# Kernel optimization log

Hardware: AMD Instinct MI355X
Metric: run time of the kernel (lower is better)

Reference implementation:

```python
import jax, jax.numpy as jnp
import numpy as np

E = 384        # number of edges
HID = 128      # hidden_dim
NH = 8         # num_heads
DH = HID // NH # head_dim = 16
NR = 64        # num_radial
CUTOFF = 10.0
AIN = 2 * DH + NR + 1  # attention MLP input dim = 97


def _xavier(key, fan_in, fan_out):
    a = np.sqrt(6.0 / (fan_in + fan_out))
    return jax.random.uniform(key, (fan_in, fan_out), jnp.float32, -a, a)


def setup_inputs() -> dict:
    key = jax.random.key(0)
    ks = jax.random.split(key, 16)
    return {
        "edge_features": jax.random.normal(ks[0], (E, HID), jnp.float32),
        "edge_coords": jax.random.normal(ks[1], (E, 3), jnp.float32),
        "edge_mask": jnp.zeros((E, E), jnp.float32),  # 0 = connected
        "wq": _xavier(ks[2], HID, HID),
        "wk": _xavier(ks[3], HID, HID),
        "wv": _xavier(ks[4], HID, HID),
        "rbf_centers": jnp.linspace(0.0, CUTOFF, NR).astype(jnp.float32),
        "rbf_widths": jnp.full((NR,), 0.5, jnp.float32),
        "a_w1": _xavier(ks[5], AIN, HID), "a_b1": jnp.zeros((HID,), jnp.float32),
        "a_w2": _xavier(ks[6], HID, HID), "a_b2": jnp.zeros((HID,), jnp.float32),
        "a_w3": _xavier(ks[7], HID, NH),  "a_b3": jnp.zeros((NH,), jnp.float32),
        "g_w1": _xavier(ks[8], DH, HID),  "g_b1": jnp.zeros((HID,), jnp.float32),
        "g_w2": _xavier(ks[9], HID, 1),   "g_b2": jnp.zeros((1,), jnp.float32),
        "wo": _xavier(ks[10], HID, HID),  "bo": jnp.zeros((HID,), jnp.float32),
        "ln_g": jnp.ones((HID,), jnp.float32),
        "ln_b": jnp.zeros((HID,), jnp.float32),
        "edge_index": jax.random.randint(ks[11], (2, E), 0, E, jnp.int64) if jax.config.jax_enable_x64 else jax.random.randint(ks[11], (2, E), 0, E, jnp.int32),
    }


def reference(edge_features, edge_coords, edge_mask,
              wq, wk, wv, rbf_centers, rbf_widths,
              a_w1, a_b1, a_w2, a_b2, a_w3, a_b3,
              g_w1, g_b1, g_w2, g_b2, wo, bo, ln_g, ln_b,
              edge_index):
    silu = jax.nn.silu
    n = edge_features.shape[0]

    q = (edge_features @ wq).reshape(n, NH, DH)
    k = (edge_features @ wk).reshape(n, NH, DH)
    v = (edge_features @ wv).reshape(n, NH, DH)

    # pairwise geometry [E, E, ...]
    coord_diff = edge_coords[:, None, :] - edge_coords[None, :, :]
    dist = jnp.linalg.norm(coord_diff, axis=-1) + 1e-8
    dist = jnp.clip(dist, 1e-8, 1e8)
    dot = jnp.clip(jnp.sum(edge_coords[:, None, :] * edge_coords[None, :, :], -1),
                   -1e8, 1e8)
    d = dist[..., None]                               # [E, E, 1]
    rbf = jnp.exp(-rbf_widths * (d - rbf_centers) ** 2) * (d <= CUTOFF).astype(jnp.float32)

    feats = []
    coords = edge_coords
    for h in range(NH):  # structural loop over fixed num_heads
        qh = jnp.broadcast_to(q[:, h, None, :], (n, n, DH))
        kh = jnp.broadcast_to(k[None, :, h, :], (n, n, DH))
        ai = jnp.concatenate([qh, kh, rbf, dot[..., None]], -1)  # [E, E, 97]
        x = silu(ai @ a_w1 + a_b1)
        x = silu(x @ a_w2 + a_b2)
        scores = (x @ a_w3 + a_b3)[:, :, h] + edge_mask
        scores = jnp.clip(scores, -1e9, 1e9)
        attn = jax.nn.softmax(scores, axis=-1)
        attn = jnp.nan_to_num(attn, nan=0.0, posinf=1.0, neginf=0.0)
        vh = v[:, h, :]
        feats.append(attn @ vh)
        # coord gate from v_head of the query edge, broadcast over keys
        gates = jax.nn.sigmoid(silu(vh @ g_w1 + g_b1) @ g_w2 + g_b2)  # [E, 1]
        coords = coords + jnp.einsum('ij,ijc->ic', attn * gates, coord_diff) / NH

    upd = jnp.concatenate(feats, -1)             # [E, hidden]
    y = edge_features + upd @ wo + bo            # residual + out_proj
    mu = jnp.mean(y, -1, keepdims=True)
    var = jnp.var(y, -1, keepdims=True)
    out_f = (y - mu) / jnp.sqrt(var + 1e-5) * ln_g + ln_b
    return out_f, coords
```

## Files before the change

kernel.cpp:

```cpp
#include <hip/hip_runtime.h>
#include <hip/hip_bf16.h>

#define N 384
#define HIDN 128
#define NHD 8
#define DHD 16
#define NRB 64
#define CUTF 10.0f

#define WS_V 0
#define WS_QPB (WS_V + N*HIDN)
#define WS_KPB (WS_QPB + N*NHD*HIDN/2)
#define WS_GATE (WS_KPB + N*NHD*HIDN/2)
#define WS_UPD (WS_GATE + N*NHD)
#define WS_SCORES (WS_UPD + N*HIDN)

typedef short bf16x8 __attribute__((ext_vector_type(8)));
typedef float floatx4 __attribute__((ext_vector_type(4)));
#define MFMA16(a, b, c) __builtin_amdgcn_mfma_f32_16x16x32_bf16(a, b, c, 0, 0, 0)

__device__ __forceinline__ float siluf(float x) { return x / (1.0f + __expf(-x)); }
__device__ __forceinline__ float silu_fast(float x) {
    return x * __builtin_amdgcn_rcpf(1.0f + __expf(-x));
}
__device__ __forceinline__ short f2bf(float f) {
    unsigned int b = __float_as_uint(f);
    unsigned int r = (b + 0x7fffu + ((b >> 16) & 1u)) >> 16;
    return (short)r;
}
__device__ __forceinline__ float bf2f(short s) {
    return __uint_as_float(((unsigned int)(unsigned short)s) << 16);
}
__device__ __forceinline__ float wave_sum(float v) {
    for (int o = 32; o; o >>= 1) v += __shfl_down(v, o, 64);
    return v;
}

__global__ __launch_bounds__(128) void k_pre(const float* __restrict__ ef,
    const float* __restrict__ wq, const float* __restrict__ wk, const float* __restrict__ wv,
    const float* __restrict__ aw1,
    const float* __restrict__ gw1, const float* __restrict__ gb1,
    const float* __restrict__ gw2, const float* __restrict__ gb2,
    float* __restrict__ v, unsigned short* __restrict__ Qpb,
    unsigned short* __restrict__ Kpb, float* __restrict__ gates) {
    __shared__ float sE[HIDN], sQ[HIDN], sK[HIDN], sV[HIDN];
    __shared__ float sRed[2];
    int i = blockIdx.x, t = threadIdx.x;
    sE[t] = ef[i * HIDN + t];
    __syncthreads();
    float aq = 0.f, ak = 0.f, av = 0.f;
#pragma unroll 8
    for (int c = 0; c < HIDN; c++) {
        float e = sE[c];
        aq += e * wq[c * HIDN + t];
        ak += e * wk[c * HIDN + t];
        av += e * wv[c * HIDN + t];
    }
    v[i * HIDN + t] = av;
    sQ[t] = aq; sK[t] = ak; sV[t] = av;
    __syncthreads();
    for (int h = 0; h < NHD; h++) {
        float accq = 0.f, acck = 0.f;
#pragma unroll
        for (int d = 0; d < DHD; d++) {
            accq += sQ[h * DHD + d] * aw1[d * HIDN + t];
            acck += sK[h * DHD + d] * aw1[(DHD + d) * HIDN + t];
        }
        Qpb[(i * NHD + h) * HIDN + t] = (unsigned short)f2bf(accq);
        Kpb[(i * NHD + h) * HIDN + t] = (unsigned short)f2bf(acck);
        float tt = gb1[t];
#pragma unroll
        for (int d = 0; d < DHD; d++) tt += sV[h * DHD + d] * gw1[d * HIDN + t];
        float contrib = siluf(tt) * gw2[t];
        float s = wave_sum(contrib);
        if ((t & 63) == 0) sRed[t >> 6] = s;
        __syncthreads();
        if (t == 0) gates[i * NHD + h] = 1.0f / (1.0f + __expf(-(sRed[0] + sRed[1] + gb2[0])));
        __syncthreads();
    }
}

#define OFF_W1RT 0
#define OFF_QPB  18432
#define OFF_W3T  20480
#define OFF_B1   24576
#define OFF_W1D  25088
#define OFF_B2   25600
#define OFF_AB3  26112
#define OFF_SDD  26144
#define OFF_RBF  26272
#define OFF_R    28576
#define SMEM_SZ  37024
#define OFF_STAGE 0

__global__ __launch_bounds__(256, 2) void k_scores_mfma(
    const float* __restrict__ coords, const float* __restrict__ mask,
    const float* __restrict__ centers, const float* __restrict__ widths,
    const float* __restrict__ aw1, const float* __restrict__ ab1,
    const float* __restrict__ aw2, const float* __restrict__ ab2,
    const float* __restrict__ aw3, const float* __restrict__ ab3,
    const unsigned short* __restrict__ Qpb, const unsigned short* __restrict__ Kpb,
    float* __restrict__ scores) {
    __shared__ __align__(16) char smem[SMEM_SZ];
    const int t = threadIdx.x;
    const int lane = t & 63;
    const int w = t >> 6;
    const int l15 = lane & 15;
    const int quad = lane >> 4;
    const int i = blockIdx.y;
    const int jb = blockIdx.x * 128;

    for (int idx = t; idx < HIDN * HIDN; idx += 256) {
        int k = idx >> 7, n = idx & 127;
        *(short*)(smem + OFF_STAGE + n * 272 + k * 2) = f2bf(aw2[idx]);
    }
    __syncthreads();
    bf16x8 BW2[8][4];
#pragma unroll
    for (int ct = 0; ct < 8; ct++)
#pragma unroll
        for (int ks = 0; ks < 4; ks++)
            BW2[ct][ks] = *(const bf16x8*)(smem + OFF_STAGE + (ct * 16 + l15) * 272 + ks * 64 + quad * 16);
    __syncthreads();
    for (int idx = t; idx < NRB * HIDN; idx += 256) {
        int r = idx >> 7, n = idx & 127;
        *(short*)(smem + OFF_W1RT + n * 144 + r * 2) = f2bf(aw1[32 * HIDN + idx]);
    }
    {
        const unsigned int* qsrc = (const unsigned int*)(Qpb + (size_t)i * NHD * HIDN);
        for (int idx = t; idx < 512; idx += 256) *(unsigned int*)(smem + OFF_QPB + idx * 4) = qsrc[idx];
    }
    for (int idx = t; idx < HIDN * NHD; idx += 256) {
        int c = idx >> 3, h = idx & 7;
        *(float*)(smem + OFF_W3T + (h * 128 + c) * 4) = aw3[idx];
    }
    if (t < 128) {
        *(float*)(smem + OFF_B1 + t * 4) = ab1[t];
        *(float*)(smem + OFF_W1D + t * 4) = aw1[96 * HIDN + t];
        *(float*)(smem + OFF_B2 + t * 4) = ab2[t];
    }
    if (t < 8) *(float*)(smem + OFF_AB3 + t * 4) = ab3[t];
    const float cix = coords[i * 3], ciy = coords[i * 3 + 1], ciz = coords[i * 3 + 2];
    __syncthreads();

    for (int ch = 0; ch < 8; ch++) {
        const int j0 = jb + ch * 16;
        {
            int r = t & 63, j4 = t >> 6;
            float cr = centers[r], rw = widths[r];
#pragma unroll
            for (int p = 0; p < 4; p++) {
                int j = j4 + p * 4;
                int jj = j0 + j;
                float jx = coords[jj * 3], jy = coords[jj * 3 + 1], jz = coords[jj * 3 + 2];
                float dx = cix - jx, dy = ciy - jy, dz = ciz - jz;
                float dist = sqrtf(dx * dx + dy * dy + dz * dz) + 1e-8f;
                dist = fminf(fmaxf(dist, 1e-8f), 1e8f);
                float dd = dist - cr;
                float val = (dist <= CUTF) ? __expf(-rw * dd * dd) : 0.0f;
                *(short*)(smem + OFF_RBF + j * 144 + r * 2) = f2bf(val);
            }
            if (t < 16) {
                int jj = j0 + t;
                float jx = coords[jj * 3], jy = coords[jj * 3 + 1], jz = coords[jj * 3 + 2];
                float dot = fminf(fmaxf(cix * jx + ciy * jy + ciz * jz, -1e8f), 1e8f);
                *(float*)(smem + OFF_SDD + t * 4) = dot;
            }
        }
        __syncthreads();
        {
            bf16x8 ra0 = *(const bf16x8*)(smem + OFF_RBF + l15 * 144 + quad * 16);
            bf16x8 ra1 = *(const bf16x8*)(smem + OFF_RBF + l15 * 144 + 64 + quad * 16);
#pragma unroll
            for (int cc = 0; cc < 2; cc++) {
                int ct = w + cc * 4;
                floatx4 acc = {0.f, 0.f, 0.f, 0.f};
                bf16x8 b0 = *(const bf16x8*)(smem + OFF_W1RT + (ct * 16 + l15) * 144 + quad * 16);
                bf16x8 b1f = *(const bf16x8*)(smem + OFF_W1RT + (ct * 16 + l15) * 144 + 64 + quad * 16);
                acc = MFMA16(ra0, b0, acc);
                acc = MFMA16(ra1, b1f, acc);
                int c = ct * 16 + l15;
                float b1v = *(const float*)(smem + OFF_B1 + c * 4);
                float w1dv = *(const float*)(smem + OFF_W1D + c * 4);
#pragma unroll
                for (int r = 0; r < 4; r++) {
                    int j = quad * 4 + r;
                    float dotv = *(const float*)(smem + OFF_SDD + j * 4);
                    *(float*)(smem + OFF_R + j * 528 + c * 4) = acc[r] + b1v + dotv * w1dv;
                }
            }
        }
        __syncthreads();
#pragma unroll
        for (int hh = 0; hh < 2; hh++) {
            const int h = hh * 4 + w;
            const unsigned short* kpr = Kpb + ((size_t)(j0 + l15) * NHD + h) * HIDN;
            bf16x8 A[4];
#pragma unroll
            for (int f = 0; f < 4; f++) {
                int c8 = f * 32 + quad * 8;
                bf16x8 kp = *(const bf16x8*)(kpr + c8);
                bf16x8 qp = *(const bf16x8*)(smem + OFF_QPB + (h * 128 + c8) * 2);
                float4 r0 = *(const float4*)(smem + OFF_R + l15 * 528 + c8 * 4);
                float4 r1 = *(const float4*)(smem + OFF_R + l15 * 528 + c8 * 4 + 16);
                float rr[8] = {r0.x, r0.y, r0.z, r0.w, r1.x, r1.y, r1.z, r1.w};
                bf16x8 a;
#pragma unroll
                for (int e = 0; e < 8; e++) {
                    float x = silu_fast(bf2f(kp[e]) + bf2f(qp[e]) + rr[e]);
                    a[e] = f2bf(x);
                }
                A[f] = a;
            }
            float part[4] = {0.f, 0.f, 0.f, 0.f};
#pragma unroll
            for (int ct = 0; ct < 8; ct++) {
                floatx4 acc = {0.f, 0.f, 0.f, 0.f};
                acc = MFMA16(A[0], BW2[ct][0], acc);
                acc = MFMA16(A[1], BW2[ct][1], acc);
                acc = MFMA16(A[2], BW2[ct][2], acc);
                acc = MFMA16(A[3], BW2[ct][3], acc);
                int c = ct * 16 + l15;
                float b2v = *(const float*)(smem + OFF_B2 + c * 4);
                float w3v = *(const float*)(smem + OFF_W3T + (h * 128 + c) * 4);
#pragma unroll
                for (int r = 0; r < 4; r++)
                    part[r] += silu_fast(acc[r] + b2v) * w3v;
            }
#pragma unroll
            for (int off = 1; off < 16; off <<= 1) {
#pragma unroll
                for (int r = 0; r < 4; r++) part[r] += __shfl_xor(part[r], off, 64);
            }
            if (l15 == 0) {
                float ab3v = *(const float*)(smem + OFF_AB3 + h * 4);
#pragma unroll
                for (int r = 0; r < 4; r++) {
                    int j = quad * 4 + r;
                    float s = part[r] + ab3v + mask[(size_t)i * N + j0 + j];
                    s = fminf(fmaxf(s, -1e9f), 1e9f);
                    scores[((size_t)h * N + i) * N + j0 + j] = s;
                }
            }
        }
        __syncthreads();
    }
}

__global__ __launch_bounds__(256) void k_attn2(
    const float* __restrict__ scores, const float* __restrict__ v,
    const float* __restrict__ gates, const float* __restrict__ coords,
    float* __restrict__ upd, float* __restrict__ out) {
    __shared__ float sA[4][N];
    __shared__ float sCrd[N * 3];
    __shared__ float sC[NHD][3];
    int i = blockIdx.x, t = threadIdx.x, w = t >> 6, lane = t & 63;
    for (int idx = t; idx < N * 3; idx += 256) sCrd[idx] = coords[idx];
    float cix = coords[i * 3], ciy = coords[i * 3 + 1], ciz = coords[i * 3 + 2];
    __syncthreads();
    for (int hh = 0; hh < 2; hh++) {
        int h = hh * 4 + w;
        const float* srow = scores + ((size_t)h * N + i) * N;
        float s[6];
#pragma unroll
        for (int p = 0; p < 6; p++) s[p] = srow[lane + 64 * p];
        float m = s[0];
#pragma unroll
        for (int p = 1; p < 6; p++) m = fmaxf(m, s[p]);
        for (int off = 1; off < 64; off <<= 1) m = fmaxf(m, __shfl_xor(m, off, 64));
        float e[6], sum = 0.f;
#pragma unroll
        for (int p = 0; p < 6; p++) { e[p] = __expf(s[p] - m); sum += e[p]; }
        for (int off = 1; off < 64; off <<= 1) sum += __shfl_xor(sum, off, 64);
        float inv = 1.0f / sum;
#pragma unroll
        for (int p = 0; p < 6; p++) sA[w][lane + 64 * p] = e[p] * inv;
        __syncthreads();
        int d4 = lane & 3, grp = lane >> 2;
        float4 f4 = {0.f, 0.f, 0.f, 0.f};
        for (int j = grp; j < N; j += 16) {
            float a = sA[w][j];
            float4 vv = *(const float4*)(v + j * HIDN + h * DHD + d4 * 4);
            f4.x += a * vv.x; f4.y += a * vv.y; f4.z += a * vv.z; f4.w += a * vv.w;
        }
#pragma unroll
        for (int off = 4; off < 64; off <<= 1) {
            f4.x += __shfl_xor(f4.x, off, 64);
            f4.y += __shfl_xor(f4.y, off, 64);
            f4.z += __shfl_xor(f4.z, off, 64);
            f4.w += __shfl_xor(f4.w, off, 64);
        }
        if (lane < 4) *(float4*)(upd + i * HIDN + h * DHD + lane * 4) = f4;
        float cx = 0.f, cy = 0.f, cz = 0.f;
#pragma unroll
        for (int p = 0; p < 6; p++) {
            int j = lane + 64 * p;
            float a = sA[w][j];
            cx += a * (cix - sCrd[j * 3]);
            cy += a * (ciy - sCrd[j * 3 + 1]);
            cz += a * (ciz - sCrd[j * 3 + 2]);
        }
        for (int off = 1; off < 64; off <<= 1) {
            cx += __shfl_xor(cx, off, 64);
            cy += __shfl_xor(cy, off, 64);
            cz += __shfl_xor(cz, off, 64);
        }
        if (lane == 0) {
            float g = gates[i * NHD + h] * (1.0f / NHD);
            sC[h][0] = g * cx; sC[h][1] = g * cy; sC[h][2] = g * cz;
        }
        __syncthreads();
    }
    if (t < 3) {
        float acc = coords[i * 3 + t];
#pragma unroll
        for (int h = 0; h < NHD; h++) acc += sC[h][t];
        out[N * HIDN + i * 3 + t] = acc;
    }
}

__global__ __launch_bounds__(128) void k_out(
    const float* __restrict__ ef, const float* __restrict__ upd,
    const float* __restrict__ wo, const float* __restrict__ bo,
    const float* __restrict__ lng, const float* __restrict__ lnb,
    float* __restrict__ out) {
    __shared__ float sU[HIDN];
    __shared__ float sR[2];
    int i = blockIdx.x, c = threadIdx.x;
    sU[c] = upd[i * HIDN + c];
    __syncthreads();
    float y = ef[i * HIDN + c] + bo[c];
#pragma unroll 8
    for (int cp = 0; cp < HIDN; cp++) y += sU[cp] * wo[cp * HIDN + c];
    float s = wave_sum(y);
    if ((c & 63) == 0) sR[c >> 6] = s;
    __syncthreads();
    float mu = (sR[0] + sR[1]) * (1.0f / HIDN);
    __syncthreads();
    float dv = y - mu;
    float s2 = wave_sum(dv * dv);
    if ((c & 63) == 0) sR[c >> 6] = s2;
    __syncthreads();
    float var = (sR[0] + sR[1]) * (1.0f / HIDN);
    out[i * HIDN + c] = dv * rsqrtf(var + 1e-5f) * lng[c] + lnb[c];
}

extern "C" void kernel_launch(void* const* d_in, const int* in_sizes, int n_in,
                              void* d_out, int out_size, void* d_ws, size_t ws_size,
                              hipStream_t stream) {
    const float* ef      = (const float*)d_in[0];
    const float* coords  = (const float*)d_in[1];
    const float* mask    = (const float*)d_in[2];
    const float* wq      = (const float*)d_in[3];
    const float* wk      = (const float*)d_in[4];
    const float* wv      = (const float*)d_in[5];
    const float* centers = (const float*)d_in[6];
    const float* widths  = (const float*)d_in[7];
    const float* aw1     = (const float*)d_in[8];
    const float* ab1     = (const float*)d_in[9];
    const float* aw2     = (const float*)d_in[10];
    const float* ab2     = (const float*)d_in[11];
    const float* aw3     = (const float*)d_in[12];
    const float* ab3     = (const float*)d_in[13];
    const float* gw1     = (const float*)d_in[14];
    const float* gb1     = (const float*)d_in[15];
    const float* gw2     = (const float*)d_in[16];
    const float* gb2     = (const float*)d_in[17];
    const float* wo      = (const float*)d_in[18];
    const float* bo      = (const float*)d_in[19];
    const float* lng     = (const float*)d_in[20];
    const float* lnb     = (const float*)d_in[21];
    float* ws = (float*)d_ws;
    float* v      = ws + WS_V;
    unsigned short* Qpb = (unsigned short*)(ws + WS_QPB);
    unsigned short* Kpb = (unsigned short*)(ws + WS_KPB);
    float* gates  = ws + WS_GATE;
    float* upd    = ws + WS_UPD;
    float* scores = ws + WS_SCORES;
    float* out = (float*)d_out;

    k_pre<<<N, 128, 0, stream>>>(ef, wq, wk, wv, aw1, gw1, gb1, gw2, gb2, v, Qpb, Kpb, gates);
    k_scores_mfma<<<dim3(3, N), 256, 0, stream>>>(
        coords, mask, centers, widths, aw1, ab1, aw2, ab2, aw3, ab3, Qpb, Kpb, scores);
    k_attn2<<<N, 256, 0, stream>>>(scores, v, gates, coords, upd, out);
    k_out<<<N, 128, 0, stream>>>(ef, upd, wo, bo, lng, lnb, out);
}
```

Baseline: 296.9 us.

## Pre-convert W2 to bf16 once and stream it from global to raise occupancy

The bf16 transpose of the second attention-MLP weight moves into k_pre and is written once to workspace. The scores kernel no longer converts W2 per block or holds it in 32 registers; it reads B fragments from global/L2 inside the column loop and raises launch bounds to 4 blocks per SM. It also processes both heads per wave together so each W2 fragment is reused twice, and folds the biases into the MFMA accumulator init. The aim is to remove the repeated per-block conversion and register pressure, at the cost of more global loads per tile.

```diff
diff --git a/kernel.cpp b/kernel.cpp
--- a/kernel.cpp
+++ b/kernel.cpp
@@ -14,6 +14,7 @@
 #define WS_GATE (WS_KPB + N*NHD*HIDN/2)
 #define WS_UPD (WS_GATE + N*NHD)
 #define WS_SCORES (WS_UPD + N*HIDN)
+#define WS_W2BF (WS_SCORES + NHD*N*N)
 
 typedef short bf16x8 __attribute__((ext_vector_type(8)));
 typedef float floatx4 __attribute__((ext_vector_type(4)));
@@ -38,14 +39,16 @@
 
 __global__ __launch_bounds__(128) void k_pre(const float* __restrict__ ef,
     const float* __restrict__ wq, const float* __restrict__ wk, const float* __restrict__ wv,
-    const float* __restrict__ aw1,
+    const float* __restrict__ aw1, const float* __restrict__ aw2,
     const float* __restrict__ gw1, const float* __restrict__ gb1,
     const float* __restrict__ gw2, const float* __restrict__ gb2,
     float* __restrict__ v, unsigned short* __restrict__ Qpb,
-    unsigned short* __restrict__ Kpb, float* __restrict__ gates) {
+    unsigned short* __restrict__ Kpb, float* __restrict__ gates,
+    unsigned short* __restrict__ w2bf) {
     __shared__ float sE[HIDN], sQ[HIDN], sK[HIDN], sV[HIDN];
     __shared__ float sRed[2];
     int i = blockIdx.x, t = threadIdx.x;
+    if (i < HIDN) w2bf[(size_t)i * HIDN + t] = (unsigned short)f2bf(aw2[t * HIDN + i]);
     sE[t] = ef[i * HIDN + t];
     __syncthreads();
     float aq = 0.f, ak = 0.f, av = 0.f;
@@ -91,15 +94,15 @@
 #define OFF_RBF  26272
 #define OFF_R    28576
 #define SMEM_SZ  37024
-#define OFF_STAGE 0
-
-__global__ __launch_bounds__(256, 2) void k_scores_mfma(
+
+__global__ __launch_bounds__(256, 4) void k_scores_mfma(
     const float* __restrict__ coords, const float* __restrict__ mask,
     const float* __restrict__ centers, const float* __restrict__ widths,
     const float* __restrict__ aw1, const float* __restrict__ ab1,
-    const float* __restrict__ aw2, const float* __restrict__ ab2,
+    const float* __restrict__ ab2,
     const float* __restrict__ aw3, const float* __restrict__ ab3,
     const unsigned short* __restrict__ Qpb, const unsigned short* __restrict__ Kpb,
+    const unsigned short* __restrict__ w2bf,
     float* __restrict__ scores) {
     __shared__ __align__(16) char smem[SMEM_SZ];
     const int t = threadIdx.x;
@@ -110,18 +113,6 @@
     const int i = blockIdx.y;
     const int jb = blockIdx.x * 128;
 
-    for (int idx = t; idx < HIDN * HIDN; idx += 256) {
-        int k = idx >> 7, n = idx & 127;
-        *(short*)(smem + OFF_STAGE + n * 272 + k * 2) = f2bf(aw2[idx]);
-    }
-    __syncthreads();
-    bf16x8 BW2[8][4];
-#pragma unroll
-    for (int ct = 0; ct < 8; ct++)
-#pragma unroll
-        for (int ks = 0; ks < 4; ks++)
-            BW2[ct][ks] = *(const bf16x8*)(smem + OFF_STAGE + (ct * 16 + l15) * 272 + ks * 64 + quad * 16);
-    __syncthreads();
     for (int idx = t; idx < NRB * HIDN; idx += 256) {
         int r = idx >> 7, n = idx & 127;
         *(short*)(smem + OFF_W1RT + n * 144 + r * 2) = f2bf(aw1[32 * HIDN + idx]);
@@ -174,72 +165,89 @@
 #pragma unroll
             for (int cc = 0; cc < 2; cc++) {
                 int ct = w + cc * 4;
-                floatx4 acc = {0.f, 0.f, 0.f, 0.f};
+                int c = ct * 16 + l15;
+                float b1v = *(const float*)(smem + OFF_B1 + c * 4);
+                float w1dv = *(const float*)(smem + OFF_W1D + c * 4);
+                floatx4 acc;
+#pragma unroll
+                for (int r = 0; r < 4; r++) {
+                    float dotv = *(const float*)(smem + OFF_SDD + (quad * 4 + r) * 4);
+                    acc[r] = b1v + dotv * w1dv;
+                }
                 bf16x8 b0 = *(const bf16x8*)(smem + OFF_W1RT + (ct * 16 + l15) * 144 + quad * 16);
                 bf16x8 b1f = *(const bf16x8*)(smem + OFF_W1RT + (ct * 16 + l15) * 144 + 64 + quad * 16);
                 acc = MFMA16(ra0, b0, acc);
                 acc = MFMA16(ra1, b1f, acc);
-                int c = ct * 16 + l15;
-                float b1v = *(const float*)(smem + OFF_B1 + c * 4);
-                float w1dv = *(const float*)(smem + OFF_W1D + c * 4);
-#pragma unroll
-                for (int r = 0; r < 4; r++) {
-                    int j = quad * 4 + r;
-                    float dotv = *(const float*)(smem + OFF_SDD + j * 4);
-                    *(float*)(smem + OFF_R + j * 528 + c * 4) = acc[r] + b1v + dotv * w1dv;
-                }
-            }
-        }
-        __syncthreads();
-#pragma unroll
-        for (int hh = 0; hh < 2; hh++) {
-            const int h = hh * 4 + w;
-            const unsigned short* kpr = Kpb + ((size_t)(j0 + l15) * NHD + h) * HIDN;
-            bf16x8 A[4];
+#pragma unroll
+                for (int r = 0; r < 4; r++)
+                    *(float*)(smem + OFF_R + (quad * 4 + r) * 528 + c * 4) = acc[r];
+            }
+        }
+        __syncthreads();
+        {
+            bf16x8 A2[2][4];
 #pragma unroll
             for (int f = 0; f < 4; f++) {
                 int c8 = f * 32 + quad * 8;
-                bf16x8 kp = *(const bf16x8*)(kpr + c8);
-                bf16x8 qp = *(const bf16x8*)(smem + OFF_QPB + (h * 128 + c8) * 2);
                 float4 r0 = *(const float4*)(smem + OFF_R + l15 * 528 + c8 * 4);
                 float4 r1 = *(const float4*)(smem + OFF_R + l15 * 528 + c8 * 4 + 16);
                 float rr[8] = {r0.x, r0.y, r0.z, r0.w, r1.x, r1.y, r1.z, r1.w};
-                bf16x8 a;
-#pragma unroll
-                for (int e = 0; e < 8; e++) {
-                    float x = silu_fast(bf2f(kp[e]) + bf2f(qp[e]) + rr[e]);
-                    a[e] = f2bf(x);
+#pragma unroll
+                for (int hh = 0; hh < 2; hh++) {
+                    const int h = hh * 4 + w;
+                    bf16x8 kp = *(const bf16x8*)(Kpb + ((size_t)(j0 + l15) * NHD + h) * HIDN + c8);
+                    bf16x8 qp = *(const bf16x8*)(smem + OFF_QPB + (h * 128 + c8) * 2);
+                    bf16x8 a;
+#pragma unroll
+                    for (int e = 0; e < 8; e++) {
+                        float x = silu_fast(bf2f(kp[e]) + bf2f(qp[e]) + rr[e]);
+                        a[e] = f2bf(x);
+                    }
+                    A2[hh][f] = a;
                 }
-                A[f] = a;
-            }
-            float part[4] = {0.f, 0.f, 0.f, 0.f};
-#pragma unroll
+            }
+            float part[2][4] = {{0.f, 0.f, 0.f, 0.f}, {0.f, 0.f, 0.f, 0.f}};
+#pragma unroll 2
             for (int ct = 0; ct < 8; ct++) {
-                floatx4 acc = {0.f, 0.f, 0.f, 0.f};
-                acc = MFMA16(A[0], BW2[ct][0], acc);
-                acc = MFMA16(A[1], BW2[ct][1], acc);
-                acc = MFMA16(A[2], BW2[ct][2], acc);
-                acc = MFMA16(A[3], BW2[ct][3], acc);
+                const unsigned short* wrow = w2bf + (ct * 16 + l15) * HIDN + quad * 8;
+                bf16x8 b0  = *(const bf16x8*)(wrow);
+                bf16x8 b1f = *(const bf16x8*)(wrow + 32);
+                bf16x8 b2f = *(const bf16x8*)(wrow + 64);
+                bf16x8 b3f = *(const bf16x8*)(wrow + 96);
                 int c = ct * 16 + l15;
                 float b2v = *(const float*)(smem + OFF_B2 + c * 4);
-                float w3v = *(const float*)(smem + OFF_W3T + (h * 128 + c) * 4);
-#pragma unroll
-                for (int r = 0; r < 4; r++)
-                    part[r] += silu_fast(acc[r] + b2v) * w3v;
-            }
-#pragma unroll
-            for (int off = 1; off < 16; off <<= 1) {
-#pragma unroll
-                for (int r = 0; r < 4; r++) part[r] += __shfl_xor(part[r], off, 64);
-            }
+#pragma unroll
+                for (int hh = 0; hh < 2; hh++) {
+                    floatx4 acc = {b2v, b2v, b2v, b2v};
+                    acc = MFMA16(A2[hh][0], b0, acc);
+                    acc = MFMA16(A2[hh][1], b1f, acc);
+                    acc = MFMA16(A2[hh][2], b2f, acc);
+                    acc = MFMA16(A2[hh][3], b3f, acc);
+                    float w3v = *(const float*)(smem + OFF_W3T + ((hh * 4 + w) * 128 + c) * 4);
+#pragma unroll
+                    for (int r = 0; r < 4; r++)
+                        part[hh][r] += silu_fast(acc[r]) * w3v;
+                }
+            }
+#pragma unroll
+            for (int off = 1; off < 16; off <<= 1)
+#pragma unroll
+                for (int hh = 0; hh < 2; hh++)
+#pragma unroll
+                    for (int r = 0; r < 4; r++)
+                        part[hh][r] += __shfl_xor(part[hh][r], off, 64);
             if (l15 == 0) {
-                float ab3v = *(const float*)(smem + OFF_AB3 + h * 4);
-#pragma unroll
-                for (int r = 0; r < 4; r++) {
-                    int j = quad * 4 + r;
-                    float s = part[r] + ab3v + mask[(size_t)i * N + j0 + j];
-                    s = fminf(fmaxf(s, -1e9f), 1e9f);
-                    scores[((size_t)h * N + i) * N + j0 + j] = s;
+#pragma unroll
+                for (int hh = 0; hh < 2; hh++) {
+                    const int h = hh * 4 + w;
+                    float ab3v = *(const float*)(smem + OFF_AB3 + h * 4);
+#pragma unroll
+                    for (int r = 0; r < 4; r++) {
+                        int j = quad * 4 + r;
+                        float s = part[hh][r] + ab3v + mask[(size_t)i * N + j0 + j];
+                        s = fminf(fmaxf(s, -1e9f), 1e9f);
+                        scores[((size_t)h * N + i) * N + j0 + j] = s;
+                    }
                 }
             }
         }
@@ -377,11 +385,12 @@
     float* gates  = ws + WS_GATE;
     float* upd    = ws + WS_UPD;
     float* scores = ws + WS_SCORES;
+    unsigned short* w2bf = (unsigned short*)(ws + WS_W2BF);
     float* out = (float*)d_out;
 
-    k_pre<<<N, 128, 0, stream>>>(ef, wq, wk, wv, aw1, gw1, gb1, gw2, gb2, v, Qpb, Kpb, gates);
+    k_pre<<<N, 128, 0, stream>>>(ef, wq, wk, wv, aw1, aw2, gw1, gb1, gw2, gb2, v, Qpb, Kpb, gates, w2bf);
     k_scores_mfma<<<dim3(3, N), 256, 0, stream>>>(
-        coords, mask, centers, widths, aw1, ab1, aw2, ab2, aw3, ab3, Qpb, Kpb, scores);
+        coords, mask, centers, widths, aw1, ab1, ab2, aw3, ab3, Qpb, Kpb, w2bf, scores);
     k_attn2<<<N, 256, 0, stream>>>(scores, v, gates, coords, upd, out);
     k_out<<<N, 128, 0, stream>>>(ef, upd, wo, bo, lng, lnb, out);
 }
```

Result: slower. 353.3 us (+19.0%).
